# Kernel optimization log

Hardware: AMD Instinct MI355X
Metric: run time of the kernel (lower is better)

Reference implementation:

```python
import jax, jax.numpy as jnp
import numpy as np


def _conv(x, w, stride, pad):
    return jax.lax.conv_general_dilated(
        x, w, (stride, stride), [(pad, pad), (pad, pad)],
        dimension_numbers=('NCHW', 'OIHW', 'NCHW'))


def _bn(x):
    m = x.mean(axis=(0, 2, 3), keepdims=True)
    v = x.var(axis=(0, 2, 3), keepdims=True)
    return (x - m) * jax.lax.rsqrt(v + 1e-5)


def _lrelu(x):
    return jnp.where(x > 0, x, 0.2 * x)


def _down(x, w):   # DownBlock: 4x4 s2 conv + norm + LeakyReLU(0.2)
    return _lrelu(_bn(_conv(x, w, 2, 1)))


def _lsb(x, w):    # LSBlock: 3x3 s1 conv + norm + LeakyReLU(0.2)
    return _lrelu(_bn(_conv(x, w, 1, 1)))


def _roi_align(feat, boxes, out=8, n=2):
    # torchvision-style roi_align, spatial_scale=1, sampling_ratio=n, aligned=False
    B, C, H, W = feat.shape
    bidx = boxes[:, 0].astype(jnp.int32)
    bx1, by1, bx2, by2 = boxes[:, 1], boxes[:, 2], boxes[:, 3], boxes[:, 4]
    rw = jnp.maximum(bx2 - bx1, 1.0)
    rh = jnp.maximum(by2 - by1, 1.0)
    S = out * n
    g = (jnp.arange(S, dtype=feat.dtype) + 0.5) / n            # sample offsets in bin units
    xs = jnp.clip(bx1[:, None] + g * (rw / out)[:, None], 0.0, W - 1)  # [K,S]
    ys = jnp.clip(by1[:, None] + g * (rh / out)[:, None], 0.0, H - 1)
    x0 = jnp.floor(xs).astype(jnp.int32)
    y0 = jnp.floor(ys).astype(jnp.int32)
    x1i = jnp.minimum(x0 + 1, W - 1)
    y1i = jnp.minimum(y0 + 1, H - 1)
    lx = xs - x0.astype(feat.dtype)
    ly = ys - y0.astype(feat.dtype)
    b = bidx[:, None, None]

    def gat(yi, xi):  # gather only the needed corner values -> [K,S,S,C]
        return feat[b, :, yi[:, :, None], xi[:, None, :]]

    w00 = ((1 - ly)[:, :, None] * (1 - lx)[:, None, :])[..., None]
    w01 = ((1 - ly)[:, :, None] * lx[:, None, :])[..., None]
    w10 = (ly[:, :, None] * (1 - lx)[:, None, :])[..., None]
    w11 = (ly[:, :, None] * lx[:, None, :])[..., None]
    val = (w00 * gat(y0, x0) + w01 * gat(y0, x1i)
           + w10 * gat(y1i, x0) + w11 * gat(y1i, x1i))       # [K,S,S,C]
    K = val.shape[0]
    val = val.reshape(K, out, n, out, n, C).mean(axis=(2, 4))  # avg over samples per bin
    return jnp.transpose(val, (0, 3, 1, 2))                    # [K,C,out,out]


def _make_boxes(key, K, B, H):
    k1, k2, k3, k4 = jax.random.split(key, 4)
    x1 = jax.random.uniform(k1, (K,), minval=0.0, maxval=H * 0.5)
    y1 = jax.random.uniform(k2, (K,), minval=0.0, maxval=H * 0.5)
    w = jax.random.uniform(k3, (K,), minval=4.0, maxval=H * 0.5)
    h = jax.random.uniform(k4, (K,), minval=4.0, maxval=H * 0.5)
    x2 = jnp.minimum(x1 + w, H - 1.0)
    y2 = jnp.minimum(y1 + h, H - 1.0)
    bidx = (jnp.arange(K) % B).astype(jnp.float32)  # every image covered
    return jnp.stack([bidx, x1, y1, x2, y2], axis=1)


def setup_inputs() -> dict:
    key = jax.random.key(0)
    ks = jax.random.split(key, 16)
    B, K = 32, 1024
    inp = {
        'feat0': jax.random.normal(ks[0], (B, 64, 64, 64), jnp.float32),
        'feat1': jax.random.normal(ks[1], (B, 128, 32, 32), jnp.float32),
        'bbox_s': _make_boxes(ks[2], K, B, 64),
        'bbox_m': _make_boxes(ks[3], K, B, 32),
        'bbox_l': _make_boxes(ks[4], K, B, 16),
        'd0_w1': jax.random.normal(ks[5], (128, 64, 4, 4), jnp.float32) * 0.05,
        'd0_w2': jax.random.normal(ks[6], (256, 128, 4, 4), jnp.float32) * 0.05,
        'd0_w3': jax.random.normal(ks[7], (512, 256, 4, 4), jnp.float32) * 0.05,
        'd0_wo': jax.random.normal(ks[8], (1, 512, 4, 4), jnp.float32) * 0.05,
        'd1_w1': jax.random.normal(ks[9], (256, 128, 4, 4), jnp.float32) * 0.05,
        'd1_w2': jax.random.normal(ks[10], (512, 256, 4, 4), jnp.float32) * 0.05,
        'd1_wo': jax.random.normal(ks[11], (1, 512, 4, 4), jnp.float32) * 0.05,
        'lsb1_w': jax.random.normal(ks[12], (128, 64, 3, 3), jnp.float32) * 0.05,
        'lsb2_w': jax.random.normal(ks[13], (128, 256, 3, 3), jnp.float32) * 0.05,
        'lsb3_w': jax.random.normal(ks[14], (128, 512, 3, 3), jnp.float32) * 0.05,
        'last_w': jax.random.normal(ks[15], (1, 128, 4, 4), jnp.float32) * 0.05,
    }
    return inp


def reference(feat0, feat1, bbox_s, bbox_m, bbox_l,
              d0_w1, d0_w2, d0_w3, d0_wo, d1_w1, d1_w2, d1_wo,
              lsb1_w, lsb2_w, lsb3_w, last_w):
    B = feat0.shape[0]
    # mini-disc 0 (start_sz=64): tap feats before each down-block
    f64 = feat0
    x = _down(feat0, d0_w1)          # [B,128,32,32]
    f32_0 = x
    x = _down(x, d0_w2)              # [B,256,16,16]
    f16_0 = x
    x = _down(x, d0_w3)              # [B,512,8,8]
    logit0 = _conv(x, d0_wo, 1, 0)   # [B,1,5,5]
    # mini-disc 1 (start_sz=32)
    f32_1 = feat1
    x = _down(feat1, d1_w1)          # [B,256,16,16]
    f16_1 = x
    x = _down(x, d1_w2)              # [B,512,8,8]
    logit1 = _conv(x, d1_wo, 1, 0)
    all_logits = jnp.concatenate([logit0, logit1], axis=1)   # [B,2,5,5]

    a64 = _lsb(f64, lsb1_w)                                   # [B,128,64,64]
    a32 = _lsb(jnp.concatenate([f32_0, f32_1], axis=1), lsb2_w)  # [B,128,32,32]
    a16 = _lsb(jnp.concatenate([f16_0, f16_1], axis=1), lsb3_w)  # [B,128,16,16]

    r64 = _roi_align(a64, bbox_s)    # [K,128,8,8]
    r32 = _roi_align(a32, bbox_m)
    r16 = _roi_align(a16, bbox_l)

    ids = jnp.concatenate([bbox_s[:, 0], bbox_m[:, 0], bbox_l[:, 0]]).astype(jnp.int32)
    all_feat = jnp.concatenate([r64, r32, r16], axis=0)       # [3K,128,8,8]
    # per-image masked mean == segment mean over batch index
    ssum = jax.ops.segment_sum(all_feat, ids, num_segments=B)
    cnt = jax.ops.segment_sum(jnp.ones((ids.shape[0],), all_feat.dtype), ids, num_segments=B)
    pooled = ssum / jnp.maximum(cnt, 1.0)[:, None, None, None]  # [B,128,8,8]
    final = _conv(pooled, last_w, 1, 0)                         # [B,1,5,5]
    return (all_logits, final)
```

## Files before the change

kernel.cpp:

```cpp
#include <hip/hip_runtime.h>
#include <cstdint>
#include <cstddef>

typedef unsigned short u16;
typedef unsigned int uint;
typedef __attribute__((ext_vector_type(8))) short short8;
typedef __attribute__((ext_vector_type(4))) float f32x4;

#define LRELU(v) ((v) > 0.f ? (v) : 0.2f * (v))

__device__ inline float b2f(u16 u) { uint x = ((uint)u) << 16; return __builtin_bit_cast(float, x); }
__device__ inline u16 f2b(float f) {
    uint x = __builtin_bit_cast(uint, f);
    uint r = (x + 0x7FFFu + ((x >> 16) & 1u)) >> 16;
    return (u16)r;
}

__device__ inline void g2l16(const void* g, void* l) {
    __builtin_amdgcn_global_load_lds((const __attribute__((address_space(1))) unsigned int*)g,
                                     (__attribute__((address_space(3))) unsigned int*)l,
                                     16, 0, 0);
}

__device__ inline void bn_ms(const float* __restrict__ bnb, int c, float invn,
                             float& m, float& rstd) {
    m = bnb[c] * invn;
    float var = fmaxf(bnb[512 + c] * invn - m * m, 0.f);
    rstd = rsqrtf(var + 1e-5f);
}

__global__ void tr_cvt_k(const float* __restrict__ in, u16* __restrict__ out, int C, int HW) {
    __shared__ float t[32][33];
    int b = blockIdx.z, c0 = blockIdx.y * 32, hw0 = blockIdx.x * 32;
    int tx = threadIdx.x & 31, ty = threadIdx.x >> 5;
    const float* ib = in + ((size_t)b * C + c0) * HW + hw0;
#pragma unroll
    for (int i = 0; i < 4; ++i)
        t[ty + 8 * i][tx] = ib[(size_t)(ty + 8 * i) * HW + tx];
    __syncthreads();
    u16* ob = out + ((size_t)b * HW + hw0) * C + c0;
#pragma unroll
    for (int i = 0; i < 4; ++i)
        ob[(size_t)(ty + 8 * i) * C + tx] = f2b(t[tx][ty + 8 * i]);
}

struct ArrangeDesc { const float* w; u16* wf; int CIN, KHW, NK, total; };
struct ArrangeArgs { ArrangeDesc d[8]; };

__global__ void arrange_all_k(ArrangeArgs a) {
    for (int seg = 0; seg < 8; ++seg) {
        const ArrangeDesc& D = a.d[seg];
        for (int i = blockIdx.x * blockDim.x + threadIdx.x; i < D.total; i += gridDim.x * blockDim.x) {
            int j = i & 7;
            int t = i >> 3;
            int lane = t & 63; t >>= 6;
            int mf = t & 7; t >>= 3;
            int ks = t % D.NK;
            int mb = t / D.NK;
            int row = mb * 128 + mf * 16 + (lane & 15);
            int k = ks * 32 + ((lane >> 4) & 3) * 8 + j;
            int rs = k / D.CIN, ci = k % D.CIN;
            D.wf[i] = f2b(D.w[((size_t)row * D.CIN + ci) * D.KHW + rs]);
        }
    }
}

template<int CINA, int CINB, int H, int W, int STR, int PAD, int KD, int KHW, int NFW, int SPLITK, int GX, int GY>
__device__ void conv_body(int rel, uint4* __restrict__ sAq, uint4* __restrict__ sBq,
                          const u16* __restrict__ inA, const u16* __restrict__ inB,
                          const u16* __restrict__ wf, u16* __restrict__ zout,
                          float* __restrict__ part, const u16* __restrict__ zpad, int Cout)
{
    constexpr int CIN = CINA + CINB;
    constexpr int K = CIN * KHW;
    constexpr int NK = K / 32;
    constexpr int NKS = NK / SPLITK;
    constexpr int HO = (H + 2 * PAD - KD) / STR + 1;
    constexpr int WO = HO;
    constexpr int HOWO = HO * WO;
    constexpr int BN = NFW * 32;
    constexpr int NFRAG = BN / 16;
    constexpr int NFF = (NFRAG + 3) / 4;
    constexpr int JW = (NFW == 1) ? 2 : 2 + NFF;

    const int tid = threadIdx.x;
    const int lane = tid & 63;
    const int wv = tid >> 6;
    const int bx = rel % GX;
    const int t2 = rel / GX;
    const int by = t2 % GY;
    const int bz = t2 / GY;
    const int m0 = by * 128;
    const int n0 = bx * BN;
    const int ks0 = bz * NKS;
    const int kgrp = lane >> 4;

    int shi0[NFF], swi0[NFF];
    const u16* bA[NFF];
    const u16* bB[NFF];
#pragma unroll
    for (int ff = 0; ff < NFF; ++ff) {
        int nf = wv + 4 * ff;
        if (nf < NFRAG) {
            int col = nf * 16 + (lane & 15);
            int n = n0 + col;
            int sb = n / HOWO;
            int rem = n % HOWO;
            shi0[ff] = (rem / WO) * STR - PAD;
            swi0[ff] = (rem % WO) * STR - PAD;
            bA[ff] = inA + (size_t)sb * H * W * CINA;
            bB[ff] = (CINB > 0) ? inB + (size_t)sb * H * W * CINB : nullptr;
        }
    }

    const uint4* wsq = (const uint4*)wf + (size_t)by * NK * 512;

    auto issue = [&](int ks, int buf) {
        const uint4* wk = wsq + (size_t)ks * 512;
        g2l16(wk + tid, &sAq[buf * 512 + wv * 64]);
        g2l16(wk + 256 + tid, &sAq[buf * 512 + 256 + wv * 64]);
        int kb = ks * 32 + kgrp * 8;
        int rs = kb / CIN;
        int ci = kb - rs * CIN;
        int r = rs / KD, s = rs - r * KD;
#pragma unroll
        for (int ff = 0; ff < NFF; ++ff) {
            int nf = wv + 4 * ff;
            if (nf < NFRAG) {
                int hi = shi0[ff] + r, wi = swi0[ff] + s;
                bool ok = ((unsigned)hi < (unsigned)H) && ((unsigned)wi < (unsigned)W);
                const u16* p;
                if (CINB > 0 && ci >= CINA)
                    p = bB[ff] + ((size_t)hi * W + wi) * CINB + (ci - CINA);
                else
                    p = bA[ff] + ((size_t)hi * W + wi) * CINA + ci;
                if (!ok) p = zpad;
                g2l16(p, &sBq[buf * 512 + nf * 64]);
            }
        }
    };

    f32x4 acc[4][NFW];
#pragma unroll
    for (int i = 0; i < 4; ++i)
#pragma unroll
        for (int j = 0; j < NFW; ++j) acc[i][j] = (f32x4){0.f, 0.f, 0.f, 0.f};

    const int mf0 = (wv >> 1) * 4;
    const int nf0 = (wv & 1) * NFW;

    issue(ks0, 0);

    for (int kk = 0; kk < NKS; ++kk) {
        const int cur = kk & 1;
        if (kk + 1 < NKS) {
            issue(ks0 + kk + 1, cur ^ 1);
            asm volatile("s_waitcnt vmcnt(%0)" :: "i"(JW) : "memory");
        } else {
            asm volatile("s_waitcnt vmcnt(0)" ::: "memory");
        }
        __builtin_amdgcn_s_barrier();
        __builtin_amdgcn_sched_barrier(0);
        short8 bfr[NFW];
#pragma unroll
        for (int j = 0; j < NFW; ++j) bfr[j] = *(const short8*)&sBq[cur * 512 + (nf0 + j) * 64 + lane];
#pragma unroll
        for (int i = 0; i < 4; ++i) {
            short8 af = *(const short8*)&sAq[cur * 512 + (mf0 + i) * 64 + lane];
#pragma unroll
            for (int j = 0; j < NFW; ++j)
                acc[i][j] = __builtin_amdgcn_mfma_f32_16x16x32_bf16(af, bfr[j], acc[i][j], 0, 0, 0);
        }
        __builtin_amdgcn_s_barrier();
    }

    const size_t NC = (size_t)GX * BN * Cout;
#pragma unroll
    for (int j = 0; j < NFW; ++j) {
        int col = n0 + (nf0 + j) * 16 + (lane & 15);
        int chb = m0 + (lane >> 4) * 4;
        if (SPLITK > 1) {
            float* pp = part + (size_t)bz * NC + (size_t)col * Cout + chb;
#pragma unroll
            for (int i = 0; i < 4; ++i)
                *(f32x4*)(pp + (mf0 + i) * 16) = acc[i][j];
        } else {
            u16* op = zout + (size_t)col * Cout + chb;
#pragma unroll
            for (int i = 0; i < 4; ++i) {
                u16 o[4];
#pragma unroll
                for (int r = 0; r < 4; ++r) o[r] = f2b(acc[i][j][r]);
                *(uint2*)(op + (mf0 + i) * 16) = *(const uint2*)o;
            }
        }
    }
}

__global__ __launch_bounds__(256) void conv_L1_k(
    const u16* f0b, const u16* f1b,
    const u16* wl1, const u16* w01, const u16* w11,
    u16* a64b, u16* x1b, u16* y1b, const u16* zpad)
{
    __shared__ uint4 smem[2048];
    int bz = blockIdx.x;
    if (bz < 1024)
        conv_body<64, 0, 64, 64, 1, 1, 3, 9, 4, 1, 1024, 1>(bz, smem, smem + 1024,
            f0b, nullptr, wl1, a64b, nullptr, zpad, 128);
    else if (bz < 1536)
        conv_body<64, 0, 64, 64, 2, 1, 4, 16, 2, 1, 512, 1>(bz - 1024, smem, smem + 1024,
            f0b, nullptr, w01, x1b, nullptr, zpad, 128);
    else
        conv_body<128, 0, 32, 32, 2, 1, 4, 16, 1, 1, 256, 2>(bz - 1536, smem, smem + 1024,
            f1b, nullptr, w11, y1b, nullptr, zpad, 256);
}

__global__ __launch_bounds__(256) void conv_L2_k(
    const u16* x1b, const u16* f1b, const u16* y1b,
    const u16* wl2, const u16* w02, const u16* w12,
    u16* a32b, u16* x2b, float* partY2, const u16* zpad)
{
    __shared__ uint4 smem[2048];
    int bz = blockIdx.x;
    if (bz < 512)
        conv_body<128, 128, 32, 32, 1, 1, 3, 9, 2, 1, 512, 1>(bz, smem, smem + 1024,
            x1b, f1b, wl2, a32b, nullptr, zpad, 128);
    else if (bz < 1024)
        conv_body<128, 0, 32, 32, 2, 1, 4, 16, 1, 1, 256, 2>(bz - 512, smem, smem + 1024,
            x1b, nullptr, w02, x2b, nullptr, zpad, 256);
    else
        conv_body<256, 0, 16, 16, 2, 1, 4, 16, 1, 4, 64, 4>(bz - 1024, smem, smem + 1024,
            y1b, nullptr, w12, nullptr, partY2, zpad, 512);
}

__global__ __launch_bounds__(256) void conv_L3_k(
    const u16* x2b, const u16* y1b,
    const u16* wl3, const u16* w03,
    float* partA16, float* partX3, const u16* zpad)
{
    __shared__ uint4 smem[2048];
    int bz = blockIdx.x;
    if (bz < 1024)
        conv_body<256, 256, 16, 16, 1, 1, 3, 9, 1, 4, 256, 1>(bz, smem, smem + 1024,
            x2b, y1b, wl3, nullptr, partA16, zpad, 128);
    else
        conv_body<256, 0, 16, 16, 2, 1, 4, 16, 1, 4, 64, 4>(bz - 1024, smem, smem + 1024,
            x2b, nullptr, w03, nullptr, partX3, zpad, 512);
}

struct RedSeg { const float* part; u16* zout; size_t n4; int S; int blkStart; int nblk; };
struct RedArgs { RedSeg s[2]; int n; };

__global__ void reduce_all_k(RedArgs a) {
    int si = (a.n > 1 && (int)blockIdx.x >= a.s[1].blkStart) ? 1 : 0;
    RedSeg S = a.s[si];
    size_t stride = (size_t)S.nblk * blockDim.x;
    for (size_t i = (size_t)(blockIdx.x - S.blkStart) * blockDim.x + threadIdx.x; i < S.n4; i += stride) {
        float4 v = ((const float4*)S.part)[i];
        for (int z = 1; z < S.S; ++z) {
            float4 b = ((const float4*)S.part)[(size_t)z * S.n4 + i];
            v.x += b.x; v.y += b.y; v.z += b.z; v.w += b.w;
        }
        u16 o[4] = { f2b(v.x), f2b(v.y), f2b(v.z), f2b(v.w) };
        ((uint2*)S.zout)[i] = *(const uint2*)o;
    }
}

struct BnpSeg { const u16* z; float* bnb; int R, C, gx, blkStart; };
struct BnpArgs { BnpSeg s[3]; int n; };

__global__ void bn_partial_all_k(BnpArgs a) {
    int si = 0;
    if (a.n > 1 && (int)blockIdx.x >= a.s[1].blkStart) si = 1;
    if (a.n > 2 && (int)blockIdx.x >= a.s[2].blkStart) si = 2;
    BnpSeg S = a.s[si];
    int rel = blockIdx.x - S.blkStart;
    int c0 = (rel / S.gx) * 64;
    int bx = rel % S.gx;
    int chg = threadIdx.x & 15;
    int rowo = threadIdx.x >> 4;
    float s[4] = {0.f, 0.f, 0.f, 0.f}, s2[4] = {0.f, 0.f, 0.f, 0.f};
    for (int r = bx * 16 + rowo; r < S.R; r += S.gx * 16) {
        uint2 v = *(const uint2*)(S.z + (size_t)r * S.C + c0 + chg * 4);
        const u16* e = (const u16*)&v;
#pragma unroll
        for (int j = 0; j < 4; ++j) { float f = b2f(e[j]); s[j] += f; s2[j] = fmaf(f, f, s2[j]); }
    }
    __shared__ float red[2][16][16][4];
#pragma unroll
    for (int j = 0; j < 4; ++j) { red[0][rowo][chg][j] = s[j]; red[1][rowo][chg][j] = s2[j]; }
    __syncthreads();
    if (threadIdx.x < 64) {
        int cg = threadIdx.x >> 2, j = threadIdx.x & 3;
        float x = 0.f, y = 0.f;
#pragma unroll
        for (int rr = 0; rr < 16; ++rr) { x += red[0][rr][cg][j]; y += red[1][rr][cg][j]; }
        atomicAdd(&S.bnb[c0 + cg * 4 + j], x);
        atomicAdd(&S.bnb[512 + c0 + cg * 4 + j], y);
    }
}

struct BnaSeg { u16* z; const float* bnb; int Cmask; float invn; size_t total8; int blkStart; int nblk; };
struct BnaArgs { BnaSeg s[3]; int n; };

__global__ void bn_act_all_k(BnaArgs a) {
    int si = 0;
    if (a.n > 1 && (int)blockIdx.x >= a.s[1].blkStart) si = 1;
    if (a.n > 2 && (int)blockIdx.x >= a.s[2].blkStart) si = 2;
    BnaSeg S = a.s[si];
    size_t stride = (size_t)S.nblk * blockDim.x;
    for (size_t i = (size_t)(blockIdx.x - S.blkStart) * blockDim.x + threadIdx.x; i < S.total8; i += stride) {
        int c0 = (int)((i * 8) & (size_t)S.Cmask);
        uint4 v = ((const uint4*)S.z)[i];
        u16* e = (u16*)&v;
        u16 o[8];
#pragma unroll
        for (int j = 0; j < 8; ++j) {
            float m, rstd;
            bn_ms(S.bnb, c0 + j, S.invn, m, rstd);
            float f = (b2f(e[j]) - m) * rstd;
            o[j] = f2b(LRELU(f));
        }
        ((uint4*)S.z)[i] = *(const uint4*)o;
    }
}

struct LogitPair { const u16* in[2]; const float* w[2]; const float* bnb[2]; float* outp; };

__global__ void logit_all_k(LogitPair lp) {
    int p = blockIdx.x, b = blockIdx.y, zi = blockIdx.z;
    int oy = p / 5, ox = p % 5;
    const int Cin = 512;
    const float invn = 1.f / (32.f * 64.f);
    const u16* inb = lp.in[zi] + (size_t)b * 64 * Cin;
    const float* w = lp.w[zi];
    const float* bnb = lp.bnb[zi];
    float acc = 0.f;
    for (int idx = threadIdx.x; idx < 16 * 64; idx += blockDim.x) {
        int cg = idx & 63;
        int rs = idx >> 6;
        int r = rs >> 2, s = rs & 3;
        int pix = (oy + r) * 8 + (ox + s);
        uint4 v = *(const uint4*)(inb + (size_t)pix * Cin + cg * 8);
        const u16* e = (const u16*)&v;
#pragma unroll
        for (int j = 0; j < 8; ++j) {
            int c = cg * 8 + j;
            float m, rstd;
            bn_ms(bnb, c, invn, m, rstd);
            float f = (b2f(e[j]) - m) * rstd;
            f = LRELU(f);
            acc = fmaf(f, w[(size_t)c * 16 + rs], acc);
        }
    }
    __shared__ float sb[4];
    for (int off = 32; off; off >>= 1) acc += __shfl_down(acc, off, 64);
    int wid = threadIdx.x >> 6, ln = threadIdx.x & 63;
    if (ln == 0) sb[wid] = acc;
    __syncthreads();
    if (threadIdx.x == 0)
        lp.outp[(size_t)b * 50 + zi * 25 + p] = sb[0] + sb[1] + sb[2] + sb[3];
}

struct RoiScale { const u16* feat; const float* boxes; float* splane; int HS; };
struct RoiAll { RoiScale s[3]; };

__global__ __launch_bounds__(256) void roi_gather_all_k(RoiAll ra) {
    int bid = blockIdx.x, pq = blockIdx.y;
    const RoiScale& S = ra.s[blockIdx.z >> 2];
    int zz = blockIdx.z & 3;
    const int HS = S.HS;
    int tid = threadIdx.x;

    __shared__ int   si0[2][8][16];
    __shared__ int   si1[2][8][16];
    __shared__ float sfl[2][8][16];
    {
        int axis = tid >> 7;
        int rem = tid & 127;
        int jj = rem >> 4, g = rem & 15;
        const float* bx = ra.s[blockIdx.z >> 2].boxes + (size_t)(bid + 32 * (zz * 8 + jj)) * 5;
        float c1 = axis ? bx[1] : bx[2];
        float c2 = axis ? bx[3] : bx[4];
        float rr = fmaxf(c2 - c1, 1.f) * 0.125f;
        float sc = ((float)g + 0.5f) * 0.5f;
        float v = fminf(fmaxf(c1 + sc * rr, 0.f), (float)(HS - 1));
        int i0 = (int)floorf(v);
        si0[axis][jj][g] = i0;
        si1[axis][jj][g] = min(i0 + 1, HS - 1);
        sfl[axis][jj][g] = v - (float)i0;
    }
    __syncthreads();

    int p = pq * 16 + (tid >> 4);
    int cg = tid & 15;
    int oy = p >> 3, ox = p & 7;
    const u16* fb = S.feat + (size_t)bid * HS * HS * 128;
    float acc[8] = {0.f, 0.f, 0.f, 0.f, 0.f, 0.f, 0.f, 0.f};
#pragma unroll 2
    for (int jj = 0; jj < 8; ++jj) {
#pragma unroll
        for (int iy = 0; iy < 2; ++iy) {
            int gy = 2 * oy + iy;
            int y0 = si0[0][jj][gy], y1i = si1[0][jj][gy];
            float ly = sfl[0][jj][gy];
            const u16* row0 = fb + (size_t)y0 * HS * 128 + cg * 8;
            const u16* row1 = fb + (size_t)y1i * HS * 128 + cg * 8;
#pragma unroll
            for (int ix = 0; ix < 2; ++ix) {
                int gx = 2 * ox + ix;
                int x0 = si0[1][jj][gx], x1i = si1[1][jj][gx];
                float lx = sfl[1][jj][gx];
                uint4 v00 = *(const uint4*)(row0 + x0 * 128);
                uint4 v01 = *(const uint4*)(row0 + x1i * 128);
                uint4 v10 = *(const uint4*)(row1 + x0 * 128);
                uint4 v11 = *(const uint4*)(row1 + x1i * 128);
                const u16* e00 = (const u16*)&v00; const u16* e01 = (const u16*)&v01;
                const u16* e10 = (const u16*)&v10; const u16* e11 = (const u16*)&v11;
                float w00 = (1.f - ly) * (1.f - lx), w01 = (1.f - ly) * lx;
                float w10 = ly * (1.f - lx), w11 = ly * lx;
#pragma unroll
                for (int q = 0; q < 8; ++q)
                    acc[q] += w00 * b2f(e00[q]) + w01 * b2f(e01[q])
                            + w10 * b2f(e10[q]) + w11 * b2f(e11[q]);
            }
        }
    }
    float* sp = S.splane + (size_t)zz * 32 * 64 * 128 + ((size_t)bid * 64 + p) * 128 + cg * 8;
#pragma unroll
    for (int q = 0; q < 8; ++q) sp[q] = acc[q] * 0.25f;
}

__global__ void final_k(const float* __restrict__ ssum, const float* __restrict__ w,
                        float* __restrict__ outp) {
    int p = blockIdx.x, b = blockIdx.y;
    int oy = p / 5, ox = p % 5;
    const float inv = 1.f / 96.f;
    const size_t plane = (size_t)32 * 64 * 128;
    const float* inb = ssum + (size_t)b * 64 * 128;
    float acc = 0.f;
    for (int idx = threadIdx.x; idx < 256; idx += blockDim.x) {
        int cg = idx & 15;
        int rs = idx >> 4;
        int r = rs >> 2, s = rs & 3;
        int pix = (oy + r) * 8 + (ox + s);
        const float* pp = inb + (size_t)pix * 128 + cg * 8;
#pragma unroll
        for (int j = 0; j < 8; ++j) {
            float v = 0.f;
#pragma unroll
            for (int q = 0; q < 12; ++q) v += pp[(size_t)q * plane + j];
            acc = fmaf(v, w[(size_t)(cg * 8 + j) * 16 + rs], acc);
        }
    }
    __shared__ float sb[4];
    for (int off = 32; off; off >>= 1) acc += __shfl_down(acc, off, 64);
    int wid = threadIdx.x >> 6, ln = threadIdx.x & 63;
    if (ln == 0) sb[wid] = acc;
    __syncthreads();
    if (threadIdx.x == 0)
        outp[(size_t)b * 25 + p] = (sb[0] + sb[1] + sb[2] + sb[3]) * inv;
}

extern "C" void kernel_launch(void* const* d_in, const int* in_sizes, int n_in,
                              void* d_out, int out_size, void* d_ws, size_t ws_size,
                              hipStream_t stream) {
    const float* feat0  = (const float*)d_in[0];
    const float* feat1  = (const float*)d_in[1];
    const float* bbox_s = (const float*)d_in[2];
    const float* bbox_m = (const float*)d_in[3];
    const float* bbox_l = (const float*)d_in[4];
    const float* d0_w1  = (const float*)d_in[5];
    const float* d0_w2  = (const float*)d_in[6];
    const float* d0_w3  = (const float*)d_in[7];
    const float* d0_wo  = (const float*)d_in[8];
    const float* d1_w1  = (const float*)d_in[9];
    const float* d1_w2  = (const float*)d_in[10];
    const float* d1_wo  = (const float*)d_in[11];
    const float* lsb1_w = (const float*)d_in[12];
    const float* lsb2_w = (const float*)d_in[13];
    const float* lsb3_w = (const float*)d_in[14];
    const float* last_w = (const float*)d_in[15];
    float* out = (float*)d_out;

    const int B = 32;

    char* wsb = (char*)d_ws;
    auto alloc = [&](size_t bytes) -> void* {
        void* p = (void*)wsb;
        wsb += (bytes + 255) & ~(size_t)255;
        return p;
    };
    u16* f0b  = (u16*)alloc((size_t)B * 64 * 64 * 64 * 2);
    u16* f1b  = (u16*)alloc((size_t)B * 32 * 32 * 128 * 2);
    u16* x1b  = (u16*)alloc((size_t)B * 32 * 32 * 128 * 2);
    u16* x2b  = (u16*)alloc((size_t)B * 16 * 16 * 256 * 2);
    u16* x3b  = (u16*)alloc((size_t)B * 8 * 8 * 512 * 2);
    u16* y1b  = (u16*)alloc((size_t)B * 16 * 16 * 256 * 2);
    u16* y2b  = (u16*)alloc((size_t)B * 8 * 8 * 512 * 2);
    u16* a64b = (u16*)alloc((size_t)B * 64 * 64 * 128 * 2);
    u16* a32b = (u16*)alloc((size_t)B * 32 * 32 * 128 * 2);
    u16* a16b = (u16*)alloc((size_t)B * 16 * 16 * 128 * 2);
    u16* wf_d0w1 = (u16*)alloc((size_t)128 * 1024 * 2);
    u16* wf_d0w2 = (u16*)alloc((size_t)256 * 2048 * 2);
    u16* wf_d0w3 = (u16*)alloc((size_t)512 * 4096 * 2);
    u16* wf_d1w1 = (u16*)alloc((size_t)256 * 2048 * 2);
    u16* wf_d1w2 = (u16*)alloc((size_t)512 * 4096 * 2);
    u16* wf_l1   = (u16*)alloc((size_t)128 * 576 * 2);
    u16* wf_l2   = (u16*)alloc((size_t)128 * 2304 * 2);
    u16* wf_l3   = (u16*)alloc((size_t)128 * 4608 * 2);
    float* ssum  = (float*)alloc((size_t)12 * B * 64 * 128 * 4);
    float* bnar  = (float*)alloc(8 * 2048 * 4);
    u16*   zpad  = (u16*)alloc(256);
    float* partA = (float*)alloc((size_t)4 * 1048576 * 4);
    float* partB = (float*)alloc((size_t)4 * 1048576 * 4);

    (void)hipMemsetAsync(bnar, 0, 8 * 2048 * 4 + 256, stream);

    hipLaunchKernelGGL(tr_cvt_k, dim3(4096 / 32, 64 / 32, B), dim3(256), 0, stream, feat0, f0b, 64, 4096);
    hipLaunchKernelGGL(tr_cvt_k, dim3(1024 / 32, 128 / 32, B), dim3(256), 0, stream, feat1, f1b, 128, 1024);

    {
        ArrangeArgs aa;
        auto mk = [](const float* w, u16* wf, int CIN, int KHW, int Cout) {
            ArrangeDesc d; d.w = w; d.wf = wf; d.CIN = CIN; d.KHW = KHW;
            d.NK = CIN * KHW / 32; d.total = Cout * CIN * KHW; return d;
        };
        aa.d[0] = mk(d0_w1, wf_d0w1, 64, 16, 128);
        aa.d[1] = mk(d0_w2, wf_d0w2, 128, 16, 256);
        aa.d[2] = mk(d0_w3, wf_d0w3, 256, 16, 512);
        aa.d[3] = mk(d1_w1, wf_d1w1, 128, 16, 256);
        aa.d[4] = mk(d1_w2, wf_d1w2, 256, 16, 512);
        aa.d[5] = mk(lsb1_w, wf_l1, 64, 9, 128);
        aa.d[6] = mk(lsb2_w, wf_l2, 256, 9, 128);
        aa.d[7] = mk(lsb3_w, wf_l3, 512, 9, 128);
        hipLaunchKernelGGL(arrange_all_k, dim3(1024), dim3(256), 0, stream, aa);
    }

    hipLaunchKernelGGL(conv_L1_k, dim3(2048), dim3(256), 0, stream,
                       f0b, f1b, wf_l1, wf_d0w1, wf_d1w1, a64b, x1b, y1b, zpad);
    {
        BnpArgs ba; ba.n = 3;
        ba.s[0] = { x1b, bnar + 0 * 2048, B * 1024, 128, 256, 0 };
        ba.s[1] = { y1b, bnar + 3 * 2048, B * 256, 256, 256, 512 };
        ba.s[2] = { a64b, bnar + 5 * 2048, B * 4096, 128, 256, 1536 };
        hipLaunchKernelGGL(bn_partial_all_k, dim3(2048), dim3(256), 0, stream, ba);
    }
    {
        BnaArgs ba; ba.n = 3;
        ba.s[0] = { x1b, bnar + 0 * 2048, 127, 1.f / 32768.f, (size_t)B * 1024 * 128 / 8, 0, 1024 };
        ba.s[1] = { y1b, bnar + 3 * 2048, 255, 1.f / 8192.f, (size_t)B * 256 * 256 / 8, 1024, 1024 };
        ba.s[2] = { a64b, bnar + 5 * 2048, 127, 1.f / 131072.f, (size_t)B * 4096 * 128 / 8, 2048, 1024 };
        hipLaunchKernelGGL(bn_act_all_k, dim3(3072), dim3(256), 0, stream, ba);
    }

    hipLaunchKernelGGL(conv_L2_k, dim3(2048), dim3(256), 0, stream,
                       x1b, f1b, y1b, wf_l2, wf_d0w2, wf_d1w2, a32b, x2b, partA, zpad);
    {
        RedArgs ra; ra.n = 1;
        ra.s[0] = { partA, y2b, (size_t)B * 64 * 512 / 4, 4, 0, 512 };
        ra.s[1] = ra.s[0];
        hipLaunchKernelGGL(reduce_all_k, dim3(512), dim3(256), 0, stream, ra);
    }
    {
        BnpArgs ba; ba.n = 3;
        ba.s[0] = { x2b, bnar + 1 * 2048, B * 256, 256, 256, 0 };
        ba.s[1] = { y2b, bnar + 4 * 2048, B * 64, 512, 128, 1024 };
        ba.s[2] = { a32b, bnar + 6 * 2048, B * 1024, 128, 256, 2048 };
        hipLaunchKernelGGL(bn_partial_all_k, dim3(2560), dim3(256), 0, stream, ba);
    }
    {
        BnaArgs ba; ba.n = 2;
        ba.s[0] = { x2b, bnar + 1 * 2048, 255, 1.f / 8192.f, (size_t)B * 256 * 256 / 8, 0, 1024 };
        ba.s[1] = { a32b, bnar + 6 * 2048, 127, 1.f / 32768.f, (size_t)B * 1024 * 128 / 8, 1024, 1024 };
        ba.s[2] = ba.s[1];
        hipLaunchKernelGGL(bn_act_all_k, dim3(2048), dim3(256), 0, stream, ba);
    }

    hipLaunchKernelGGL(conv_L3_k, dim3(2048), dim3(256), 0, stream,
                       x2b, y1b, wf_l3, wf_d0w3, partB, partA, zpad);
    {
        RedArgs ra; ra.n = 2;
        ra.s[0] = { partB, a16b, (size_t)B * 256 * 128 / 4, 4, 0, 512 };
        ra.s[1] = { partA, x3b, (size_t)B * 64 * 512 / 4, 4, 512, 512 };
        hipLaunchKernelGGL(reduce_all_k, dim3(1024), dim3(256), 0, stream, ra);
    }
    {
        BnpArgs ba; ba.n = 2;
        ba.s[0] = { x3b, bnar + 2 * 2048, B * 64, 512, 128, 0 };
        ba.s[1] = { a16b, bnar + 7 * 2048, B * 256, 128, 256, 1024 };
        ba.s[2] = ba.s[1];
        hipLaunchKernelGGL(bn_partial_all_k, dim3(1536), dim3(256), 0, stream, ba);
    }
    {
        BnaArgs ba; ba.n = 1;
        ba.s[0] = { a16b, bnar + 7 * 2048, 127, 1.f / 8192.f, (size_t)B * 256 * 128 / 8, 0, 512 };
        ba.s[1] = ba.s[0]; ba.s[2] = ba.s[0];
        hipLaunchKernelGGL(bn_act_all_k, dim3(512), dim3(256), 0, stream, ba);
    }

    {
        LogitPair lp;
        lp.in[0] = x3b; lp.in[1] = y2b;
        lp.w[0] = d0_wo; lp.w[1] = d1_wo;
        lp.bnb[0] = bnar + 2 * 2048; lp.bnb[1] = bnar + 4 * 2048;
        lp.outp = out;
        hipLaunchKernelGGL(logit_all_k, dim3(25, B, 2), dim3(256), 0, stream, lp);
    }

    {
        const size_t plane4 = (size_t)4 * B * 64 * 128;
        RoiAll ra;
        ra.s[0] = { a64b, bbox_s, ssum,              64 };
        ra.s[1] = { a32b, bbox_m, ssum + plane4,     32 };
        ra.s[2] = { a16b, bbox_l, ssum + 2 * plane4, 16 };
        hipLaunchKernelGGL(roi_gather_all_k, dim3(B, 4, 12), dim3(256), 0, stream, ra);
    }

    hipLaunchKernelGGL(final_k, dim3(25, B), dim3(256), 0, stream, ssum, last_w, out + 1600);
}
```

Before: 376.3 us.

## Fuse batch-norm statistic accumulation into conv epilogues via atomics

Conv bodies gain a FUSEBN template flag that reduces per-channel sum and sum-of-squares from the fp32 accumulators with wave shuffles, then atomically adds them into the BN buffer. This removes the separate bn_partial passes after layers 1 and 2 and their re-reads of the conv outputs. The layer-3 partial launch now also covers y2b. Atomic contention and statistics computed from unrounded fp32 values rather than stored bf16 are the trade-offs, and the buffers must be zeroed beforehand.

```diff
diff --git a/kernel.cpp b/kernel.cpp
--- a/kernel.cpp
+++ b/kernel.cpp
@@ -65,11 +65,12 @@
     }
 }
 
-template<int CINA, int CINB, int H, int W, int STR, int PAD, int KD, int KHW, int NFW, int SPLITK, int GX, int GY>
+template<int CINA, int CINB, int H, int W, int STR, int PAD, int KD, int KHW, int NFW, int SPLITK, int GX, int GY, int FUSEBN>
 __device__ void conv_body(int rel, uint4* __restrict__ sAq, uint4* __restrict__ sBq,
                           const u16* __restrict__ inA, const u16* __restrict__ inB,
                           const u16* __restrict__ wf, u16* __restrict__ zout,
-                          float* __restrict__ part, const u16* __restrict__ zpad, int Cout)
+                          float* __restrict__ part, const u16* __restrict__ zpad,
+                          float* __restrict__ bnb, int Cout)
 {
     constexpr int CIN = CINA + CINB;
     constexpr int K = CIN * KHW;
@@ -195,42 +196,76 @@
             }
         }
     }
+
+    if (FUSEBN) {
+        float s1[4][4], s2[4][4];
+#pragma unroll
+        for (int i = 0; i < 4; ++i)
+#pragma unroll
+            for (int r = 0; r < 4; ++r) {
+                float a = 0.f, b = 0.f;
+#pragma unroll
+                for (int j = 0; j < NFW; ++j) { float v = acc[i][j][r]; a += v; b = fmaf(v, v, b); }
+                s1[i][r] = a; s2[i][r] = b;
+            }
+#pragma unroll
+        for (int off = 1; off < 16; off <<= 1)
+#pragma unroll
+            for (int i = 0; i < 4; ++i)
+#pragma unroll
+                for (int r = 0; r < 4; ++r) {
+                    s1[i][r] += __shfl_xor(s1[i][r], off, 64);
+                    s2[i][r] += __shfl_xor(s2[i][r], off, 64);
+                }
+        if ((lane & 15) == 0) {
+#pragma unroll
+            for (int i = 0; i < 4; ++i)
+#pragma unroll
+                for (int r = 0; r < 4; ++r) {
+                    int c = m0 + (mf0 + i) * 16 + (lane >> 4) * 4 + r;
+                    atomicAdd(&bnb[c], s1[i][r]);
+                    atomicAdd(&bnb[512 + c], s2[i][r]);
+                }
+        }
+    }
 }
 
 __global__ __launch_bounds__(256) void conv_L1_k(
     const u16* f0b, const u16* f1b,
     const u16* wl1, const u16* w01, const u16* w11,
-    u16* a64b, u16* x1b, u16* y1b, const u16* zpad)
+    u16* a64b, u16* x1b, u16* y1b, const u16* zpad,
+    float* bnA64, float* bnX1, float* bnY1)
 {
     __shared__ uint4 smem[2048];
     int bz = blockIdx.x;
     if (bz < 1024)
-        conv_body<64, 0, 64, 64, 1, 1, 3, 9, 4, 1, 1024, 1>(bz, smem, smem + 1024,
-            f0b, nullptr, wl1, a64b, nullptr, zpad, 128);
+        conv_body<64, 0, 64, 64, 1, 1, 3, 9, 4, 1, 1024, 1, 1>(bz, smem, smem + 1024,
+            f0b, nullptr, wl1, a64b, nullptr, zpad, bnA64, 128);
     else if (bz < 1536)
-        conv_body<64, 0, 64, 64, 2, 1, 4, 16, 2, 1, 512, 1>(bz - 1024, smem, smem + 1024,
-            f0b, nullptr, w01, x1b, nullptr, zpad, 128);
+        conv_body<64, 0, 64, 64, 2, 1, 4, 16, 2, 1, 512, 1, 1>(bz - 1024, smem, smem + 1024,
+            f0b, nullptr, w01, x1b, nullptr, zpad, bnX1, 128);
     else
-        conv_body<128, 0, 32, 32, 2, 1, 4, 16, 1, 1, 256, 2>(bz - 1536, smem, smem + 1024,
-            f1b, nullptr, w11, y1b, nullptr, zpad, 256);
+        conv_body<128, 0, 32, 32, 2, 1, 4, 16, 1, 1, 256, 2, 1>(bz - 1536, smem, smem + 1024,
+            f1b, nullptr, w11, y1b, nullptr, zpad, bnY1, 256);
 }
 
 __global__ __launch_bounds__(256) void conv_L2_k(
     const u16* x1b, const u16* f1b, const u16* y1b,
     const u16* wl2, const u16* w02, const u16* w12,
-    u16* a32b, u16* x2b, float* partY2, const u16* zpad)
+    u16* a32b, u16* x2b, float* partY2, const u16* zpad,
+    float* bnA32, float* bnX2)
 {
     __shared__ uint4 smem[2048];
     int bz = blockIdx.x;
     if (bz < 512)
-        conv_body<128, 128, 32, 32, 1, 1, 3, 9, 2, 1, 512, 1>(bz, smem, smem + 1024,
-            x1b, f1b, wl2, a32b, nullptr, zpad, 128);
+        conv_body<128, 128, 32, 32, 1, 1, 3, 9, 2, 1, 512, 1, 1>(bz, smem, smem + 1024,
+            x1b, f1b, wl2, a32b, nullptr, zpad, bnA32, 128);
     else if (bz < 1024)
-        conv_body<128, 0, 32, 32, 2, 1, 4, 16, 1, 1, 256, 2>(bz - 512, smem, smem + 1024,
-            x1b, nullptr, w02, x2b, nullptr, zpad, 256);
+        conv_body<128, 0, 32, 32, 2, 1, 4, 16, 1, 1, 256, 2, 1>(bz - 512, smem, smem + 1024,
+            x1b, nullptr, w02, x2b, nullptr, zpad, bnX2, 256);
     else
-        conv_body<256, 0, 16, 16, 2, 1, 4, 16, 1, 4, 64, 4>(bz - 1024, smem, smem + 1024,
-            y1b, nullptr, w12, nullptr, partY2, zpad, 512);
+        conv_body<256, 0, 16, 16, 2, 1, 4, 16, 1, 4, 64, 4, 0>(bz - 1024, smem, smem + 1024,
+            y1b, nullptr, w12, nullptr, partY2, zpad, nullptr, 512);
 }
 
 __global__ __launch_bounds__(256) void conv_L3_k(
@@ -241,11 +276,11 @@
     __shared__ uint4 smem[2048];
     int bz = blockIdx.x;
     if (bz < 1024)
-        conv_body<256, 256, 16, 16, 1, 1, 3, 9, 1, 4, 256, 1>(bz, smem, smem + 1024,
-            x2b, y1b, wl3, nullptr, partA16, zpad, 128);
+        conv_body<256, 256, 16, 16, 1, 1, 3, 9, 1, 4, 256, 1, 0>(bz, smem, smem + 1024,
+            x2b, y1b, wl3, nullptr, partA16, zpad, nullptr, 128);
     else
-        conv_body<256, 0, 16, 16, 2, 1, 4, 16, 1, 4, 64, 4>(bz - 1024, smem, smem + 1024,
-            x2b, nullptr, w03, nullptr, partX3, zpad, 512);
+        conv_body<256, 0, 16, 16, 2, 1, 4, 16, 1, 4, 64, 4, 0>(bz - 1024, smem, smem + 1024,
+            x2b, nullptr, w03, nullptr, partX3, zpad, nullptr, 512);
 }
 
 struct RedSeg { const float* part; u16* zout; size_t n4; int S; int blkStart; int nblk; };
@@ -538,14 +573,8 @@
     }
 
     hipLaunchKernelGGL(conv_L1_k, dim3(2048), dim3(256), 0, stream,
-                       f0b, f1b, wf_l1, wf_d0w1, wf_d1w1, a64b, x1b, y1b, zpad);
-    {
-        BnpArgs ba; ba.n = 3;
-        ba.s[0] = { x1b, bnar + 0 * 2048, B * 1024, 128, 256, 0 };
-        ba.s[1] = { y1b, bnar + 3 * 2048, B * 256, 256, 256, 512 };
-        ba.s[2] = { a64b, bnar + 5 * 2048, B * 4096, 128, 256, 1536 };
-        hipLaunchKernelGGL(bn_partial_all_k, dim3(2048), dim3(256), 0, stream, ba);
-    }
+                       f0b, f1b, wf_l1, wf_d0w1, wf_d1w1, a64b, x1b, y1b, zpad,
+                       bnar + 5 * 2048, bnar + 0 * 2048, bnar + 3 * 2048);
     {
         BnaArgs ba; ba.n = 3;
         ba.s[0] = { x1b, bnar + 0 * 2048, 127, 1.f / 32768.f, (size_t)B * 1024 * 128 / 8, 0, 1024 };
@@ -555,19 +584,13 @@
     }
 
     hipLaunchKernelGGL(conv_L2_k, dim3(2048), dim3(256), 0, stream,
-                       x1b, f1b, y1b, wf_l2, wf_d0w2, wf_d1w2, a32b, x2b, partA, zpad);
+                       x1b, f1b, y1b, wf_l2, wf_d0w2, wf_d1w2, a32b, x2b, partA, zpad,
+                       bnar + 6 * 2048, bnar + 1 * 2048);
     {
         RedArgs ra; ra.n = 1;
         ra.s[0] = { partA, y2b, (size_t)B * 64 * 512 / 4, 4, 0, 512 };
         ra.s[1] = ra.s[0];
         hipLaunchKernelGGL(reduce_all_k, dim3(512), dim3(256), 0, stream, ra);
-    }
-    {
-        BnpArgs ba; ba.n = 3;
-        ba.s[0] = { x2b, bnar + 1 * 2048, B * 256, 256, 256, 0 };
-        ba.s[1] = { y2b, bnar + 4 * 2048, B * 64, 512, 128, 1024 };
-        ba.s[2] = { a32b, bnar + 6 * 2048, B * 1024, 128, 256, 2048 };
-        hipLaunchKernelGGL(bn_partial_all_k, dim3(2560), dim3(256), 0, stream, ba);
     }
     {
         BnaArgs ba; ba.n = 2;
@@ -586,11 +609,11 @@
         hipLaunchKernelGGL(reduce_all_k, dim3(1024), dim3(256), 0, stream, ra);
     }
     {
-        BnpArgs ba; ba.n = 2;
-        ba.s[0] = { x3b, bnar + 2 * 2048, B * 64, 512, 128, 0 };
-        ba.s[1] = { a16b, bnar + 7 * 2048, B * 256, 128, 256, 1024 };
-        ba.s[2] = ba.s[1];
-        hipLaunchKernelGGL(bn_partial_all_k, dim3(1536), dim3(256), 0, stream, ba);
+        BnpArgs ba; ba.n = 3;
+        ba.s[0] = { y2b, bnar + 4 * 2048, B * 64, 512, 128, 0 };
+        ba.s[1] = { x3b, bnar + 2 * 2048, B * 64, 512, 128, 1024 };
+        ba.s[2] = { a16b, bnar + 7 * 2048, B * 256, 128, 256, 2048 };
+        hipLaunchKernelGGL(bn_partial_all_k, dim3(2560), dim3(256), 0, stream, ba);
     }
     {
         BnaArgs ba; ba.n = 1;
```

New measurement: 705.3 us. 87.5% more time.
